# Optimization experiments

Measured on AMD Instinct MI355X. Metric: run time of the kernel, lower is better.

## Reference

```python
import jax, jax.numpy as jnp
import numpy as np

H = 1024      # hidden_size
NH = 16       # num_heads
HD = H // NH  # head_dim
MLP_DIM = 4096
EPS = 1e-6


def setup_inputs() -> dict:
    key = jax.random.key(0)
    ks = jax.random.split(key, 16)
    B, S = 8, 1024
    s_in = 1.0 / np.sqrt(H)
    s_mlp = 1.0 / np.sqrt(MLP_DIM)
    return {
        "x": jax.random.normal(ks[0], (B, S, H), jnp.float32),
        "ln1_g": jnp.ones((H,), jnp.float32),
        "ln1_b": jnp.zeros((H,), jnp.float32),
        "Wq": jax.random.normal(ks[1], (H, H), jnp.float32) * s_in,
        "bq": jnp.zeros((H,), jnp.float32),
        "Wk": jax.random.normal(ks[2], (H, H), jnp.float32) * s_in,
        "bk": jnp.zeros((H,), jnp.float32),
        "Wv": jax.random.normal(ks[3], (H, H), jnp.float32) * s_in,
        "bv": jnp.zeros((H,), jnp.float32),
        "Wo": jax.random.normal(ks[4], (H, H), jnp.float32) * s_in,
        "bo": jnp.zeros((H,), jnp.float32),
        "ln2_g": jnp.ones((H,), jnp.float32),
        "ln2_b": jnp.zeros((H,), jnp.float32),
        "W1": jax.random.normal(ks[5], (H, MLP_DIM), jnp.float32) * s_in,
        "b1": jnp.zeros((MLP_DIM,), jnp.float32),
        "W2": jax.random.normal(ks[6], (MLP_DIM, H), jnp.float32) * s_mlp,
        "b2": jnp.zeros((H,), jnp.float32),
    }


def _layernorm(x, g, b):
    mu = jnp.mean(x, axis=-1, keepdims=True)
    var = jnp.mean(jnp.square(x - mu), axis=-1, keepdims=True)
    return (x - mu) * jax.lax.rsqrt(var + EPS) * g + b


def reference(x, ln1_g, ln1_b, Wq, bq, Wk, bk, Wv, bv, Wo, bo,
              ln2_g, ln2_b, W1, b1, W2, b2):
    B, S, _ = x.shape
    # pre-LN attention
    h = _layernorm(x, ln1_g, ln1_b)
    q = (h @ Wq + bq).reshape(B, S, NH, HD).transpose(0, 2, 1, 3)  # bhsd
    k = (h @ Wk + bk).reshape(B, S, NH, HD).transpose(0, 2, 1, 3)
    v = (h @ Wv + bv).reshape(B, S, NH, HD).transpose(0, 2, 1, 3)
    scale = HD ** -0.5
    scores = jnp.einsum('bhqd,bhkd->bhqk', q, k) * scale
    weights = jax.nn.softmax(scores, axis=-1)
    attended = jnp.einsum('bhqk,bhkd->bhqd', weights, v)
    attended = attended.transpose(0, 2, 1, 3).reshape(B, S, H)
    x = x + attended @ Wo + bo
    # pre-LN MLP
    h = _layernorm(x, ln2_g, ln2_b)
    h = jax.nn.gelu(h @ W1 + b1, approximate=False)
    x = x + h @ W2 + b2
    return x
```

## Files before the change

### kernel.cpp

```cpp
#include <hip/hip_runtime.h>

#define H_DIM 1024
#define NHEADS 16
#define HD 64
#define SEQ 1024
#define BATCH 8
#define ROWS (BATCH*SEQ)
#define MLPD 4096

typedef __bf16 bf16x8 __attribute__((ext_vector_type(8)));
typedef float f32x4 __attribute__((ext_vector_type(4)));

__device__ __forceinline__ unsigned short f2bf(float f) {
    unsigned u = __float_as_uint(f);
    unsigned r = u + 0x7FFFu + ((u >> 16) & 1u);
    return (unsigned short)(r >> 16);
}

__global__ void transpose_w(const float* __restrict__ in, unsigned short* __restrict__ out,
                            int K, int N)
{
    __shared__ float tile[32][33];
    const int n0 = blockIdx.x * 32, k0 = blockIdx.y * 32;
    const int tx = threadIdx.x, ty = threadIdx.y;
    #pragma unroll
    for (int i = ty; i < 32; i += 8)
        tile[i][tx] = in[(size_t)(k0 + i) * N + n0 + tx];
    __syncthreads();
    #pragma unroll
    for (int i = ty; i < 32; i += 8)
        out[(size_t)(n0 + i) * K + k0 + tx] = f2bf(tile[tx][i]);
}

__global__ void transpose_v(const unsigned short* __restrict__ in,
                            unsigned short* __restrict__ out)
{
    __shared__ unsigned short tile[32][33];
    const size_t base = (size_t)blockIdx.z * (SEQ * HD);
    const int d0 = blockIdx.x * 32, s0 = blockIdx.y * 32;
    const int tx = threadIdx.x, ty = threadIdx.y;
    #pragma unroll
    for (int i = ty; i < 32; i += 8)
        tile[i][tx] = in[base + (size_t)(s0 + i) * HD + d0 + tx];
    __syncthreads();
    const int fx = ((tx & 12) << 1) | ((tx & 16) >> 2) | (tx & 3);
    #pragma unroll
    for (int i = ty; i < 32; i += 8)
        out[base + (size_t)(d0 + i) * SEQ + s0 + fx] = tile[tx][i];
}

__global__ __launch_bounds__(256) void ln_kernel(const float* __restrict__ x,
    const float* __restrict__ g, const float* __restrict__ b,
    unsigned short* __restrict__ out)
{
    __shared__ float red[4];
    const int row = blockIdx.x;
    const int tid = threadIdx.x;
    const float4 v = *(const float4*)(x + (size_t)row * H_DIM + tid * 4);
    float s = v.x + v.y + v.z + v.w;
    #pragma unroll
    for (int off = 32; off >= 1; off >>= 1) s += __shfl_xor(s, off);
    if ((tid & 63) == 0) red[tid >> 6] = s;
    __syncthreads();
    const float mu = (red[0] + red[1] + red[2] + red[3]) * (1.0f / H_DIM);
    __syncthreads();
    const float dx = v.x - mu, dy = v.y - mu, dz = v.z - mu, dw = v.w - mu;
    float q = dx * dx + dy * dy + dz * dz + dw * dw;
    #pragma unroll
    for (int off = 32; off >= 1; off >>= 1) q += __shfl_xor(q, off);
    if ((tid & 63) == 0) red[tid >> 6] = q;
    __syncthreads();
    const float var = (red[0] + red[1] + red[2] + red[3]) * (1.0f / H_DIM);
    const float rstd = rsqrtf(var + 1e-6f);
    const float4 gv = *(const float4*)(g + tid * 4);
    const float4 bv = *(const float4*)(b + tid * 4);
    ushort4 o;
    o.x = f2bf(dx * rstd * gv.x + bv.x);
    o.y = f2bf(dy * rstd * gv.y + bv.y);
    o.z = f2bf(dz * rstd * gv.z + bv.z);
    o.w = f2bf(dw * rstd * gv.w + bv.w);
    *(ushort4*)(out + (size_t)row * H_DIM + tid * 4) = o;
}

template<int MODE>
__global__ __launch_bounds__(256) void gemm_dp(
    const unsigned short* __restrict__ A, const unsigned short* __restrict__ Bt,
    const float* __restrict__ bias0, const float* __restrict__ bias1,
    const float* __restrict__ bias2, const float* resid,
    float* outF, unsigned short* __restrict__ outH,
    int N, int K, int gn)
{
    __shared__ __align__(16) unsigned short As[128 * 64];
    __shared__ __align__(16) unsigned short Bs[128 * 64];

    const int tid = threadIdx.x, lane = tid & 63;
    const int w = tid >> 6;
    const int wm = w >> 1, wn = w & 1;

    const int nwg = gridDim.x;
    const int swzb = (blockIdx.x & 7) * (nwg >> 3) + (blockIdx.x >> 3);
    const int bm = swzb / gn, bn = swzb % gn;

    const int srow = tid >> 3;
    const int sc = (tid & 7) ^ (srow & 7);
    const unsigned short* Abase = A  + (size_t)(bm * 128) * K;
    const unsigned short* Bbase = Bt + (size_t)(bn * 128) * K;

    auto stage = [&](int kt) {
        const size_t kofs = (size_t)kt * 64 + sc * 8;
        #pragma unroll
        for (int q = 0; q < 4; ++q)
            __builtin_amdgcn_global_load_lds(
                (__attribute__((address_space(1))) void*)(Abase + (size_t)(q * 32 + srow) * K + kofs),
                (__attribute__((address_space(3))) void*)(&As[q * 2048 + tid * 8]), 16, 0, 0);
        #pragma unroll
        for (int q = 0; q < 4; ++q)
            __builtin_amdgcn_global_load_lds(
                (__attribute__((address_space(1))) void*)(Bbase + (size_t)(q * 32 + srow) * K + kofs),
                (__attribute__((address_space(3))) void*)(&Bs[q * 2048 + tid * 8]), 16, 0, 0);
    };

    const int lr = lane & 15, hk = lane >> 4;
    const int px0 = (hk ^ (lr & 7)) * 8;
    const int px1 = px0 ^ 32;
    const int arow = (wm * 64 + lr) * 64;
    const int brow = (wn * 64 + lr) * 64;

    f32x4 acc[4][4] = {};
    const int nkt = K >> 6;

    for (int t = 0; t < nkt; ++t) {
        stage(t);
        __syncthreads();

        const unsigned short* Ab = &As[arow];
        const unsigned short* Bb = &Bs[brow];

        bf16x8 a0[4], b0[4], a1[4], b1[4];
        #pragma unroll
        for (int i = 0; i < 4; ++i) { b0[i] = *(const bf16x8*)(Bb + i * 1024 + px0);
                                      a0[i] = *(const bf16x8*)(Ab + i * 1024 + px0); }
        #pragma unroll
        for (int i = 0; i < 4; ++i) { b1[i] = *(const bf16x8*)(Bb + i * 1024 + px1);
                                      a1[i] = *(const bf16x8*)(Ab + i * 1024 + px1); }
        __builtin_amdgcn_s_setprio(1);
        #pragma unroll
        for (int mi = 0; mi < 4; ++mi)
            #pragma unroll
            for (int ni = 0; ni < 4; ++ni)
                acc[mi][ni] = __builtin_amdgcn_mfma_f32_16x16x32_bf16(a0[mi], b0[ni], acc[mi][ni], 0, 0, 0);
        __builtin_amdgcn_s_setprio(0);
        __builtin_amdgcn_s_setprio(1);
        #pragma unroll
        for (int mi = 0; mi < 4; ++mi)
            #pragma unroll
            for (int ni = 0; ni < 4; ++ni)
                acc[mi][ni] = __builtin_amdgcn_mfma_f32_16x16x32_bf16(a1[mi], b1[ni], acc[mi][ni], 0, 0, 0);
        __builtin_amdgcn_s_setprio(0);
        __syncthreads();
    }

    #pragma unroll
    for (int mi = 0; mi < 4; ++mi) {
        #pragma unroll
        for (int ni = 0; ni < 4; ++ni) {
            const int gcol = bn * 128 + wn * 64 + ni * 16 + lr;
            #pragma unroll
            for (int r = 0; r < 4; ++r) {
                const int grow = bm * 128 + wm * 64 + mi * 16 + hk * 4 + r;
                if (MODE == 0) {
                    const int which = gcol >> 10;
                    const int col = gcol & 1023;
                    const float* bp = (which == 0) ? bias0 : (which == 1) ? bias1 : bias2;
                    const float v = acc[mi][ni][r] + bp[col];
                    const int b_ = grow >> 10, s_ = grow & 1023, h_ = col >> 6, d_ = col & 63;
                    outH[(size_t)which * (ROWS * 1024) +
                         (size_t)(b_ * NHEADS + h_) * 65536 + s_ * 64 + d_] = f2bf(v);
                } else if (MODE == 2) {
                    const float v = acc[mi][ni][r] + bias0[gcol];
                    const size_t idx = (size_t)grow * N + gcol;
                    outF[idx] = resid[idx] + v;
                } else {
                    const float v = acc[mi][ni][r] + bias0[gcol];
                    const float t3 = fmaf(0.044715f * v * v, v, v);
                    const float e  = __builtin_amdgcn_exp2f(-2.3022086f * t3);
                    const float ge = v * __builtin_amdgcn_rcpf(1.0f + e);
                    outH[(size_t)grow * N + gcol] = f2bf(ge);
                }
            }
        }
    }
}

__global__ __launch_bounds__(256) void attn_kernel(const unsigned short* __restrict__ q,
    const unsigned short* __restrict__ k, const unsigned short* __restrict__ vT,
    unsigned short* __restrict__ out)
{
    __shared__ __align__(16) unsigned short Ks[2][4096];
    __shared__ __align__(16) unsigned short Vs[2][4096];
    const int tid = threadIdx.x, lane = tid & 63, w = tid >> 6;
    const int bh = blockIdx.y;
    const int q0 = blockIdx.x * 64;
    const size_t headBase = (size_t)bh * (SEQ * HD);

    const int qrow = q0 + w * 16 + (lane & 15);
    const unsigned short* qp = q + headBase + (size_t)qrow * HD + (lane >> 4) * 8;
    const bf16x8 qf0 = *(const bf16x8*)(qp);
    const bf16x8 qf1 = *(const bf16x8*)(qp + 32);

    float lacc = 0.f;
    f32x4 oacc[4] = {};

    const int srow = tid >> 3;
    const int swz  = ((tid & 7) ^ (srow & 7)) * 8;
    const int pc   = (lane >> 4) ^ (lane & 7);

    auto stage = [&](int buf, int kt) {
        #pragma unroll
        for (int s = 0; s < 2; ++s) {
            const unsigned short* gk = k  + headBase + (size_t)(kt + s * 32 + srow) * HD + swz;
            const unsigned short* gv = vT + headBase + (size_t)(s * 32 + srow) * SEQ + kt + swz;
            __builtin_amdgcn_global_load_lds((__attribute__((address_space(1))) void*)gk,
                (__attribute__((address_space(3))) void*)(&Ks[buf][s * 2048 + w * 512]), 16, 0, 0);
            __builtin_amdgcn_global_load_lds((__attribute__((address_space(1))) void*)gv,
                (__attribute__((address_space(3))) void*)(&Vs[buf][s * 2048 + w * 512]), 16, 0, 0);
        }
    };

    stage(0, 0);
    __syncthreads();

    const float C1 = 0.125f * 1.44269504f;
    const float C2 = -4.0f * 1.44269504f;

    for (int t = 0; t < 16; ++t) {
        const int cur = t & 1;
        if (t < 15) stage(cur ^ 1, (t + 1) * 64);

        const unsigned short* KB = &Ks[cur][0];
        const unsigned short* VB = &Vs[cur][0];

        f32x4 s4[4] = {};
        #pragma unroll
        for (int ni = 0; ni < 4; ++ni) {
            const unsigned short* pk = KB + (ni * 16 + (lane & 15)) * 64;
            s4[ni] = __builtin_amdgcn_mfma_f32_16x16x32_bf16(*(const bf16x8*)(pk + pc * 8),       qf0, s4[ni], 0, 0, 0);
            s4[ni] = __builtin_amdgcn_mfma_f32_16x16x32_bf16(*(const bf16x8*)(pk + (pc ^ 4) * 8), qf1, s4[ni], 0, 0, 0);
        }

        unsigned U[4][2];
        float ls = 0.f;
        #pragma unroll
        for (int ni = 0; ni < 4; ++ni) {
            const float p0 = __builtin_amdgcn_exp2f(fmaf(s4[ni][0], C1, C2));
            const float p1 = __builtin_amdgcn_exp2f(fmaf(s4[ni][1], C1, C2));
            const float p2 = __builtin_amdgcn_exp2f(fmaf(s4[ni][2], C1, C2));
            const float p3 = __builtin_amdgcn_exp2f(fmaf(s4[ni][3], C1, C2));
            ls += (p0 + p1) + (p2 + p3);
            asm("v_cvt_pk_bf16_f32 %0, %1, %2" : "=v"(U[ni][0]) : "v"(p0), "v"(p1));
            asm("v_cvt_pk_bf16_f32 %0, %1, %2" : "=v"(U[ni][1]) : "v"(p2), "v"(p3));
        }
        lacc += ls;

        union { unsigned u[4]; bf16x8 v; } W0, W1;
        W0.u[0] = U[0][0]; W0.u[1] = U[0][1]; W0.u[2] = U[1][0]; W0.u[3] = U[1][1];
        W1.u[0] = U[2][0]; W1.u[1] = U[2][1]; W1.u[2] = U[3][0]; W1.u[3] = U[3][1];

        #pragma unroll
        for (int nd = 0; nd < 4; ++nd) {
            const unsigned short* pv = VB + (nd * 16 + (lane & 15)) * 64;
            oacc[nd] = __builtin_amdgcn_mfma_f32_16x16x32_bf16(*(const bf16x8*)(pv + pc * 8),       W0.v, oacc[nd], 0, 0, 0);
            oacc[nd] = __builtin_amdgcn_mfma_f32_16x16x32_bf16(*(const bf16x8*)(pv + (pc ^ 4) * 8), W1.v, oacc[nd], 0, 0, 0);
        }

        __syncthreads();
    }

    float l = lacc;
    l += __shfl_xor(l, 16);
    l += __shfl_xor(l, 32);
    const float inv = 1.0f / l;

    const int b_ = bh >> 4, h_ = bh & 15;
    const int s_ = q0 + w * 16 + (lane & 15);
    const int hh = (lane >> 4) * 4;
    #pragma unroll
    for (int nd = 0; nd < 4; ++nd) {
        ushort4 o;
        o.x = f2bf(oacc[nd][0] * inv);
        o.y = f2bf(oacc[nd][1] * inv);
        o.z = f2bf(oacc[nd][2] * inv);
        o.w = f2bf(oacc[nd][3] * inv);
        *(ushort4*)(out + (size_t)(b_ * SEQ + s_) * H_DIM + h_ * 64 + nd * 16 + hh) = o;
    }
}

extern "C" void kernel_launch(void* const* d_in, const int* in_sizes, int n_in,
                              void* d_out, int out_size, void* d_ws, size_t ws_size,
                              hipStream_t stream)
{
    const float* x    = (const float*)d_in[0];
    const float* ln1g = (const float*)d_in[1];
    const float* ln1b = (const float*)d_in[2];
    const float* Wq   = (const float*)d_in[3];
    const float* bq   = (const float*)d_in[4];
    const float* Wk   = (const float*)d_in[5];
    const float* bk   = (const float*)d_in[6];
    const float* Wv   = (const float*)d_in[7];
    const float* bv   = (const float*)d_in[8];
    const float* Wo   = (const float*)d_in[9];
    const float* bo   = (const float*)d_in[10];
    const float* ln2g = (const float*)d_in[11];
    const float* ln2b = (const float*)d_in[12];
    const float* W1   = (const float*)d_in[13];
    const float* b1   = (const float*)d_in[14];
    const float* W2   = (const float*)d_in[15];
    const float* b2   = (const float*)d_in[16];
    float* out = (float*)d_out;

    char* ws = (char*)d_ws;
    const size_t MB = 1024 * 1024;
    unsigned short* h1  = (unsigned short*)(ws);
    unsigned short* qb  = (unsigned short*)(ws + 16 * MB);
    unsigned short* kb  = (unsigned short*)(ws + 32 * MB);
    unsigned short* vb  = (unsigned short*)(ws + 48 * MB);
    unsigned short* vTb = (unsigned short*)(ws + 64 * MB);
    unsigned short* mlp = (unsigned short*)(ws + 16 * MB);
    unsigned short* ao  = h1;
    unsigned short* WqT = (unsigned short*)(ws + 80 * MB);
    unsigned short* WkT = (unsigned short*)(ws + 82 * MB);
    unsigned short* WvT = (unsigned short*)(ws + 84 * MB);
    unsigned short* WoT = (unsigned short*)(ws + 86 * MB);
    unsigned short* W1T = (unsigned short*)(ws + 88 * MB);
    unsigned short* W2T = (unsigned short*)(ws + 96 * MB);

    const dim3 tb(32, 8);
    transpose_w<<<dim3(32, 32),  tb, 0, stream>>>(Wq, WqT, 1024, 1024);
    transpose_w<<<dim3(32, 32),  tb, 0, stream>>>(Wk, WkT, 1024, 1024);
    transpose_w<<<dim3(32, 32),  tb, 0, stream>>>(Wv, WvT, 1024, 1024);
    transpose_w<<<dim3(32, 32),  tb, 0, stream>>>(Wo, WoT, 1024, 1024);
    transpose_w<<<dim3(128, 32), tb, 0, stream>>>(W1, W1T, 1024, 4096);
    transpose_w<<<dim3(32, 128), tb, 0, stream>>>(W2, W2T, 4096, 1024);

    ln_kernel<<<ROWS, 256, 0, stream>>>(x, ln1g, ln1b, h1);

    gemm_dp<0><<<1536, 256, 0, stream>>>(h1, WqT, bq, bk, bv, nullptr, nullptr, qb, 3072, 1024, 24);

    transpose_v<<<dim3(2, 32, 128), tb, 0, stream>>>(vb, vTb);

    attn_kernel<<<dim3(16, 128), 256, 0, stream>>>(qb, kb, vTb, ao);

    gemm_dp<2><<<512, 256, 0, stream>>>(ao, WoT, bo, bo, bo, x, out, nullptr, 1024, 1024, 8);

    ln_kernel<<<ROWS, 256, 0, stream>>>(out, ln2g, ln2b, h1);

    gemm_dp<3><<<2048, 256, 0, stream>>>(h1, W1T, b1, b1, b1, nullptr, nullptr, mlp, 4096, 1024, 32);
    gemm_dp<2><<<512, 256, 0, stream>>>(mlp, W2T, b2, b2, b2, out, out, nullptr, 1024, 4096, 8);
}
```

Baseline: 375.4 us.

## Add 256x256-tile 8-wave GEMM kernel for the W1 GELU projection

Replaces the 128x128-tile GEMM used for the MLP up-projection (with GELU epilogue) by a new kernel using 256x256 tiles, 512 threads (8 waves), and double-buffered direct global-to-LDS loads with an XOR-swizzled layout. It also uses an XCD-aware block remap and s_setprio around the MFMA bursts. The aim is higher arithmetic intensity and fewer global reloads per FLOP on the largest GEMM. In exchange it uses 128KB LDS and many accumulator registers, which limits occupancy to one block per CU and leaves only 512 blocks across the device.

```diff
diff --git a/kernel.cpp b/kernel.cpp
--- a/kernel.cpp
+++ b/kernel.cpp
@@ -180,13 +180,113 @@
                     const float v = acc[mi][ni][r] + bias0[gcol];
                     const size_t idx = (size_t)grow * N + gcol;
                     outF[idx] = resid[idx] + v;
-                } else {
-                    const float v = acc[mi][ni][r] + bias0[gcol];
-                    const float t3 = fmaf(0.044715f * v * v, v, v);
-                    const float e  = __builtin_amdgcn_exp2f(-2.3022086f * t3);
-                    const float ge = v * __builtin_amdgcn_rcpf(1.0f + e);
-                    outH[(size_t)grow * N + gcol] = f2bf(ge);
                 }
+            }
+        }
+    }
+}
+
+__global__ __launch_bounds__(512) void gemm8p(
+    const unsigned short* __restrict__ A, const unsigned short* __restrict__ Bt,
+    const float* __restrict__ bias, unsigned short* __restrict__ outH,
+    int N, int K, int gn)
+{
+    __shared__ __align__(16) unsigned short As[2][16384];
+    __shared__ __align__(16) unsigned short Bs[2][16384];
+
+    const int tid = threadIdx.x, lane = tid & 63;
+    const int w = tid >> 6;
+    const int wm = w >> 2, wn = w & 3;
+
+    const int nwg = gridDim.x;
+    const int swzb = (blockIdx.x & 7) * (nwg >> 3) + (blockIdx.x >> 3);
+    const int bm = swzb / gn, bn = swzb % gn;
+
+    const int srow = tid >> 3;
+    const int sc   = tid & 7;
+    const unsigned short* Abase = A  + (size_t)(bm * 256) * K;
+    const unsigned short* Bbase = Bt + (size_t)(bn * 256) * K;
+
+    auto stageHalf = [&](int buf, int kt, int q) {
+        const unsigned short* gb = (q >= 2) ? Bbase : Abase;
+        unsigned short* lb = ((q >= 2) ? &Bs[buf][0] : &As[buf][0]) + (q & 1) * 8192;
+        #pragma unroll
+        for (int j = 0; j < 2; ++j) {
+            const int row = srow + j * 64;
+            __builtin_amdgcn_global_load_lds(
+                (__attribute__((address_space(1))) void*)(gb
+                    + (size_t)((q & 1) * 128 + row) * K + (size_t)kt * 64
+                    + ((sc ^ (row & 7)) * 8)),
+                (__attribute__((address_space(3))) void*)(lb + j * 4096 + tid * 8), 16, 0, 0);
+        }
+    };
+
+    const int lr = lane & 15, hk = lane >> 4;
+    const int swz0 = (hk ^ (lr & 7)) * 8;
+    const int swz1 = swz0 ^ 32;
+
+    f32x4 acc[8][4] = {};
+    const int nkt = K >> 6;
+
+    stageHalf(0, 0, 0); stageHalf(0, 0, 1); stageHalf(0, 0, 2); stageHalf(0, 0, 3);
+
+    for (int t = 0; t < nkt; ++t) {
+        const int cur = t & 1, nxt = cur ^ 1;
+        bf16x8 bfr[4][2];
+        #pragma unroll
+        for (int q = 0; q < 4; ++q) {
+            if (t + 1 < nkt) stageHalf(nxt, t + 1, q);
+            if (q == 0) {
+                if (t + 1 < nkt) asm volatile("s_waitcnt vmcnt(2)" ::: "memory");
+                else             asm volatile("s_waitcnt vmcnt(0)" ::: "memory");
+            }
+            __builtin_amdgcn_s_barrier();
+            asm volatile("" ::: "memory");
+            if (q == 0) {
+                const unsigned short* Bb = &Bs[cur][(wn >> 1) * 8192 + (wn & 1) * 4096];
+                #pragma unroll
+                for (int ni = 0; ni < 4; ++ni) {
+                    const unsigned short* p = Bb + (ni * 16 + lr) * 64;
+                    bfr[ni][0] = *(const bf16x8*)(p + swz0);
+                    bfr[ni][1] = *(const bf16x8*)(p + swz1);
+                }
+            }
+            bf16x8 afr[2][2];
+            const unsigned short* Ab = &As[cur][wm * 8192];
+            #pragma unroll
+            for (int m2 = 0; m2 < 2; ++m2) {
+                const unsigned short* p = Ab + ((q * 2 + m2) * 16 + lr) * 64;
+                afr[m2][0] = *(const bf16x8*)(p + swz0);
+                afr[m2][1] = *(const bf16x8*)(p + swz1);
+            }
+            __builtin_amdgcn_s_setprio(1);
+            #pragma unroll
+            for (int ks = 0; ks < 2; ++ks)
+                #pragma unroll
+                for (int m2 = 0; m2 < 2; ++m2)
+                    #pragma unroll
+                    for (int ni = 0; ni < 4; ++ni)
+                        acc[q * 2 + m2][ni] = __builtin_amdgcn_mfma_f32_16x16x32_bf16(
+                            afr[m2][ks], bfr[ni][ks], acc[q * 2 + m2][ni], 0, 0, 0);
+            __builtin_amdgcn_s_setprio(0);
+            __builtin_amdgcn_s_barrier();
+            asm volatile("" ::: "memory");
+        }
+    }
+
+    #pragma unroll
+    for (int mf = 0; mf < 8; ++mf) {
+        #pragma unroll
+        for (int ni = 0; ni < 4; ++ni) {
+            const int gcol = bn * 256 + wn * 64 + ni * 16 + lr;
+            #pragma unroll
+            for (int r = 0; r < 4; ++r) {
+                const int grow = bm * 256 + wm * 128 + mf * 16 + hk * 4 + r;
+                const float v = acc[mf][ni][r] + bias[gcol];
+                const float t3 = fmaf(0.044715f * v * v, v, v);
+                const float e  = __builtin_amdgcn_exp2f(-2.3022086f * t3);
+                const float ge = v * __builtin_amdgcn_rcpf(1.0f + e);
+                outH[(size_t)grow * N + gcol] = f2bf(ge);
             }
         }
     }
@@ -354,6 +454,6 @@
 
     ln_kernel<<<ROWS, 256, 0, stream>>>(out, ln2g, ln2b, h1);
 
-    gemm_dp<3><<<2048, 256, 0, stream>>>(h1, W1T, b1, b1, b1, nullptr, nullptr, mlp, 4096, 1024, 32);
+    gemm8p<<<512, 512, 0, stream>>>(h1, W1T, b1, mlp, 4096, 1024, 16);
     gemm_dp<2><<<512, 256, 0, stream>>>(mlp, W2T, b2, b2, b2, out, out, nullptr, 1024, 4096, 8);
 }
```

Result: slower. 395.8 us (+5.4%).
